# Performance work log

Hardware: AMD Instinct MI355X
Metric: run time of the kernel (lower is better)

Reference implementation:

```python
import jax, jax.numpy as jnp
import numpy as np

D_MODEL = 1024
N_HEADS = 16
HEAD_DIM = D_MODEL // N_HEADS
SEQ_LEN = 2048
BATCH = 4


def setup_inputs() -> dict:
    key = jax.random.key(0)
    k1, k2, k3 = jax.random.split(key, 3)
    x = jax.random.normal(k1, (BATCH, SEQ_LEN, D_MODEL), dtype=jnp.float32)
    # Linear weights stored as [in, out] so y = x @ W (equivalent to torch x @ W.T)
    w_qkv = jax.random.normal(k2, (D_MODEL, 3 * D_MODEL), dtype=jnp.float32) * (D_MODEL ** -0.5)
    w_proj = jax.random.normal(k3, (D_MODEL, D_MODEL), dtype=jnp.float32) * (D_MODEL ** -0.5)
    return {"x": x, "w_qkv": w_qkv, "w_proj": w_proj}


def reference(x, w_qkv, w_proj):
    B, T, C = x.shape
    qkv = x @ w_qkv  # [B, T, 3C]
    q, k, v = jnp.split(qkv, 3, axis=-1)
    # [B, H, T, hd]
    q = q.reshape(B, T, N_HEADS, HEAD_DIM).transpose(0, 2, 1, 3)
    k = k.reshape(B, T, N_HEADS, HEAD_DIM).transpose(0, 2, 1, 3)
    v = v.reshape(B, T, N_HEADS, HEAD_DIM).transpose(0, 2, 1, 3)
    scale = HEAD_DIM ** -0.5
    attn = jnp.einsum("bhqd,bhkd->bhqk", q, k) * scale  # [B, H, T, T]
    causal = jnp.tril(jnp.ones((T, T), dtype=bool))
    attn = jnp.where(causal, attn, -jnp.inf)
    attn = jax.nn.softmax(attn, axis=-1)
    out = jnp.einsum("bhqk,bhkd->bhqd", attn, v)  # [B, H, T, hd]
    out = out.transpose(0, 2, 1, 3).reshape(B, T, C)
    return out @ w_proj
```

## Files before the change

kernel.cpp:

```cpp
#include <hip/hip_runtime.h>
#include <stdint.h>


typedef __bf16 bf16x8 __attribute__((ext_vector_type(8)));
typedef float f32x4 __attribute__((ext_vector_type(4)));
typedef unsigned short u16x8 __attribute__((ext_vector_type(8)));

#define DEVINL static __device__ __forceinline__

DEVINL unsigned short f2b(float f) {
  __bf16 h = (__bf16)f;
  return __builtin_bit_cast(unsigned short, h);
}

DEVINL void gld16(const void* g, void* l) {
  __builtin_amdgcn_global_load_lds(
      (const __attribute__((address_space(1))) void*)g,
      (__attribute__((address_space(3))) void*)l, 16, 0, 0);
}

DEVINL f32x4 mfma16(bf16x8 a, bf16x8 b, f32x4 c) {
  return __builtin_amdgcn_mfma_f32_16x16x32_bf16(a, b, c, 0, 0, 0);
}

#define SCHED_FENCE() __builtin_amdgcn_sched_barrier(0)

__global__ __launch_bounds__(256) void k_cast_bf16(const float* __restrict__ in,
                                                   unsigned short* __restrict__ out,
                                                   int n8) {
  int i = blockIdx.x * 256 + threadIdx.x;
  if (i >= n8) return;
  const float4* p = (const float4*)in + (size_t)i * 2;
  float4 a = p[0], b = p[1];
  u16x8 o;
  o[0] = f2b(a.x); o[1] = f2b(a.y); o[2] = f2b(a.z); o[3] = f2b(a.w);
  o[4] = f2b(b.x); o[5] = f2b(b.y); o[6] = f2b(b.z); o[7] = f2b(b.w);
  *(u16x8*)(out + (size_t)i * 8) = o;
}

__global__ __launch_bounds__(256) void k_transpose_w(const float* __restrict__ in,
                                                     unsigned short* __restrict__ out,
                                                     int R, int C) {
  __shared__ float t[64][65];
  int ci = blockIdx.x * 64, ri = blockIdx.y * 64;
  int tid = threadIdx.x;
#pragma unroll
  for (int j = 0; j < 4; ++j) {
    int c = tid + j * 256;
    int row = c >> 4;
    int col = (c & 15) * 4;
    float4 v = *(const float4*)(in + (size_t)(ri + row) * C + ci + col);
    t[row][col] = v.x; t[row][col + 1] = v.y; t[row][col + 2] = v.z; t[row][col + 3] = v.w;
  }
  __syncthreads();
  int cc = tid >> 2;
  int seg = (tid & 3) * 16;
  u16x8 o0, o1;
#pragma unroll
  for (int j = 0; j < 8; ++j) o0[j] = f2b(t[seg + j][cc]);
#pragma unroll
  for (int j = 0; j < 8; ++j) o1[j] = f2b(t[seg + 8 + j][cc]);
  unsigned short* dst = out + (size_t)(ci + cc) * R + ri + seg;
  *(u16x8*)dst = o0;
  *(u16x8*)(dst + 8) = o1;
}

__global__ __launch_bounds__(512, 4)
void k_gemmQKV(const unsigned short* __restrict__ A,
               const unsigned short* __restrict__ Bt,
               unsigned short* __restrict__ qo,
               unsigned short* __restrict__ ko,
               unsigned short* __restrict__ vo,
               float qscale) {
  const int K = 1024, N = 3072;
  __shared__ unsigned short As[3][256 * 32];
  __shared__ unsigned short Bs[3][128 * 32];
  int tid = threadIdx.x;
  int w = tid >> 6, lane = tid & 63, l15 = lane & 15, l4 = lane >> 4;
  int nwg = gridDim.x;
  int gx = N >> 7;
  int lin = blockIdx.x;
  int nx = nwg >> 3, rr = nwg & 7;
  int xcd = lin & 7, idx = lin >> 3;
  int wgid = (xcd < rr ? xcd * (nx + 1) : rr * (nx + 1) + (xcd - rr) * nx) + idx;
  int bn = wgid % gx, bm = wgid / gx;
  int wr = (w >> 1) * 64, wc = (w & 1) * 64;
  f32x4 acc[4][4];
#pragma unroll
  for (int i = 0; i < 4; ++i)
#pragma unroll
    for (int j = 0; j < 4; ++j) acc[i][j] = (f32x4){0.f, 0.f, 0.f, 0.f};
  const char* Ab = (const char*)(A + (size_t)bm * 256 * K);
  const char* Bb = (const char*)(Bt + (size_t)bn * 128 * K);
  const size_t Kb2 = (size_t)K * 2;
  int LbA0 = tid * 16, LbA1 = (tid + 512) * 16, LbB = tid * 16;
  int NA0 = LbA0 ^ (((LbA0 >> 7) & 3) << 4);
  int NA1 = LbA1 ^ (((LbA1 >> 7) & 3) << 4);
  int NB  = LbB  ^ (((LbB  >> 7) & 3) << 4);
  int rA0 = NA0 >> 6, oA0 = NA0 & 63;
  int rA1 = NA1 >> 6, oA1 = NA1 & 63;
  int rB  = NB  >> 6, oB  = NB  & 63;

  auto stage = [&](int kt, int buf) {
    gld16(Ab + (size_t)rA0 * Kb2 + kt * 2 + oA0, (char*)As[buf] + LbA0);
    gld16(Ab + (size_t)rA1 * Kb2 + kt * 2 + oA1, (char*)As[buf] + LbA1);
    gld16(Bb + (size_t)rB  * Kb2 + kt * 2 + oB,  (char*)Bs[buf] + LbB);
  };

  const int nkt = K >> 5;
  stage(0, 0);
  stage(32, 1);
  SCHED_FENCE();
  for (int t = 0; t < nkt; ++t) {
    int cur = t - (t / 3) * 3;
    if (t) {
      SCHED_FENCE();
      __builtin_amdgcn_s_barrier();
      SCHED_FENCE();
    }
    if (t + 2 < nkt) {
      int nb = (t + 2) - ((t + 2) / 3) * 3;
      stage((t + 2) * 32, nb);
      SCHED_FENCE();
      asm volatile("s_waitcnt vmcnt(6)" ::: "memory");
    } else if (t + 1 < nkt) {
      SCHED_FENCE();
      asm volatile("s_waitcnt vmcnt(3)" ::: "memory");
    } else {
      SCHED_FENCE();
      asm volatile("s_waitcnt vmcnt(0)" ::: "memory");
    }
    SCHED_FENCE();
    __builtin_amdgcn_s_barrier();
    SCHED_FENCE();
    const char* Ac = (const char*)As[cur];
    const char* Bc = (const char*)Bs[cur];
    bf16x8 af[4], bfr[4];
#pragma unroll
    for (int m = 0; m < 4; ++m) {
      int nat = (wr + m * 16 + l15) * 64 + l4 * 16;
      af[m] = *(const bf16x8*)(Ac + (nat ^ (((nat >> 7) & 3) << 4)));
    }
#pragma unroll
    for (int n = 0; n < 4; ++n) {
      int nat = (wc + n * 16 + l15) * 64 + l4 * 16;
      bfr[n] = *(const bf16x8*)(Bc + (nat ^ (((nat >> 7) & 3) << 4)));
    }
    __builtin_amdgcn_s_setprio(1);
#pragma unroll
    for (int m = 0; m < 4; ++m)
#pragma unroll
      for (int n = 0; n < 4; ++n)
        acc[m][n] = mfma16(af[m], bfr[n], acc[m][n]);
    __builtin_amdgcn_s_setprio(0);
  }
#pragma unroll
  for (int m = 0; m < 4; ++m) {
    int grow0 = bm * 256 + wr + m * 16 + l4 * 4;
#pragma unroll
    for (int n = 0; n < 4; ++n) {
      int gcol = bn * 128 + wc + n * 16 + l15;
      int which = gcol >> 10, rem = gcol & 1023;
      int h = rem >> 6, d = rem & 63;
      int b = grow0 >> 11, t0 = grow0 & 2047;
      if (which == 2) {
        uint32_t lo = (uint32_t)f2b(acc[m][n][0]) | ((uint32_t)f2b(acc[m][n][1]) << 16);
        uint32_t hi = (uint32_t)f2b(acc[m][n][2]) | ((uint32_t)f2b(acc[m][n][3]) << 16);
        size_t off = (((size_t)(b * 16 + h)) * 64 + d) * 2048 + t0;
        *(uint2*)(vo + off) = make_uint2(lo, hi);
      } else {
        size_t off = (((size_t)(b * 16 + h)) * 2048 + t0) * 64 + d;
#pragma unroll
        for (int r = 0; r < 4; ++r) {
          float val = acc[m][n][r];
          if (which == 0) qo[off + (size_t)r * 64] = f2b(val * qscale);
          else            ko[off + (size_t)r * 64] = f2b(val);
        }
      }
    }
  }
}

__global__ __launch_bounds__(256) void k_gemm_out(const unsigned short* __restrict__ A,
                                                  const unsigned short* __restrict__ Bt,
                                                  int M, int N, int K,
                                                  float* __restrict__ Cf) {
  __shared__ unsigned short As[3][128 * 32];
  __shared__ unsigned short Bs[3][128 * 32];
  int tid = threadIdx.x;
  int w = tid >> 6, lane = tid & 63, l15 = lane & 15, l4 = lane >> 4;
  int nwg = gridDim.x;
  int gx = N >> 7;
  int lin = blockIdx.x;
  int nx = nwg >> 3, rr = nwg & 7;
  int xcd = lin & 7, idx = lin >> 3;
  int wgid = (xcd < rr ? xcd * (nx + 1) : rr * (nx + 1) + (xcd - rr) * nx) + idx;
  int bn = wgid % gx, bm = wgid / gx;
  int wr = (w >> 1) * 64, wc = (w & 1) * 64;
  f32x4 acc[4][4];
#pragma unroll
  for (int i = 0; i < 4; ++i)
#pragma unroll
    for (int j = 0; j < 4; ++j) acc[i][j] = (f32x4){0.f, 0.f, 0.f, 0.f};
  const char* Ab = (const char*)(A + (size_t)bm * 128 * K);
  const char* Bb = (const char*)(Bt + (size_t)bn * 128 * K);
  int Lb0 = tid * 16, Lb1 = (tid + 256) * 16;
  int Nb0 = Lb0 ^ (((Lb0 >> 7) & 3) << 4);
  int Nb1 = Lb1 ^ (((Lb1 >> 7) & 3) << 4);
  int rA0 = Nb0 >> 6, o0 = Nb0 & 63;
  int rA1 = Nb1 >> 6, o1 = Nb1 & 63;

  auto stage = [&](int kt, int buf) {
    gld16(Ab + ((size_t)rA0 * K + kt) * 2 + o0, (char*)As[buf] + Lb0);
    gld16(Bb + ((size_t)rA0 * K + kt) * 2 + o0, (char*)Bs[buf] + Lb0);
    gld16(Ab + ((size_t)rA1 * K + kt) * 2 + o1, (char*)As[buf] + Lb1);
    gld16(Bb + ((size_t)rA1 * K + kt) * 2 + o1, (char*)Bs[buf] + Lb1);
  };

  const int nkt = K >> 5;
  stage(0, 0);
  stage(32, 1);
  SCHED_FENCE();
  for (int t = 0; t < nkt; ++t) {
    int cur = t - (t / 3) * 3;
    if (t) {
      SCHED_FENCE();
      __builtin_amdgcn_s_barrier();
      SCHED_FENCE();
    }
    if (t + 2 < nkt) {
      int nb = (t + 2) - ((t + 2) / 3) * 3;
      stage((t + 2) * 32, nb);
      SCHED_FENCE();
      asm volatile("s_waitcnt vmcnt(8)" ::: "memory");
    } else if (t + 1 < nkt) {
      SCHED_FENCE();
      asm volatile("s_waitcnt vmcnt(4)" ::: "memory");
    } else {
      SCHED_FENCE();
      asm volatile("s_waitcnt vmcnt(0)" ::: "memory");
    }
    SCHED_FENCE();
    __builtin_amdgcn_s_barrier();
    SCHED_FENCE();
    const char* Ac = (const char*)As[cur];
    const char* Bc = (const char*)Bs[cur];
    bf16x8 af[4], bfr[4];
#pragma unroll
    for (int m = 0; m < 4; ++m) {
      int nat = (wr + m * 16 + l15) * 64 + l4 * 16;
      af[m] = *(const bf16x8*)(Ac + (nat ^ (((nat >> 7) & 3) << 4)));
    }
#pragma unroll
    for (int n = 0; n < 4; ++n) {
      int nat = (wc + n * 16 + l15) * 64 + l4 * 16;
      bfr[n] = *(const bf16x8*)(Bc + (nat ^ (((nat >> 7) & 3) << 4)));
    }
    __builtin_amdgcn_s_setprio(1);
#pragma unroll
    for (int m = 0; m < 4; ++m)
#pragma unroll
      for (int n = 0; n < 4; ++n)
        acc[m][n] = mfma16(af[m], bfr[n], acc[m][n]);
    __builtin_amdgcn_s_setprio(0);
  }
#pragma unroll
  for (int m = 0; m < 4; ++m) {
    int grow0 = bm * 128 + wr + m * 16 + l4 * 4;
#pragma unroll
    for (int n = 0; n < 4; ++n) {
      int gcol = bn * 128 + wc + n * 16 + l15;
#pragma unroll
      for (int r = 0; r < 4; ++r)
        Cf[(size_t)(grow0 + r) * N + gcol] = acc[m][n][r];
    }
  }
}

__global__ __launch_bounds__(512) void k_attn(const unsigned short* __restrict__ Q,
                                              const unsigned short* __restrict__ Kt,
                                              const unsigned short* __restrict__ Vt,
                                              unsigned short* __restrict__ AO) {
  __shared__ unsigned short Ks[2][4096];
  __shared__ unsigned short Vs[2][4096];
  __shared__ unsigned short Ps[8192];
  int tid = threadIdx.x;
  int w = tid >> 6, lane = tid & 63, l15 = lane & 15, l4 = lane >> 4;
  int lin = blockIdx.x;
  int xcd = lin & 7, jj = lin >> 3;
  int bh = xcd * 8 + (jj & 7);
  int p = jj >> 3;
  const char* Kb = (const char*)(Kt + (size_t)bh * 2048 * 64);
  const char* Vb = (const char*)(Vt + (size_t)bh * 64 * 2048);
  const int swp = (l15 & 7) << 4;
  char* Pw = (char*)Ps + w * 2048;
  int b = bh >> 4, h = bh & 15;

  int Lb0 = tid * 16;
  int Nb0 = Lb0 ^ (((Lb0 >> 7) & 7) << 4);
  int d0 = Nb0 >> 7, in0 = Nb0 & 127;

  auto stage = [&](int t, int buf) {
    size_t kv0 = (size_t)t * 64;
    gld16(Kb + kv0 * 128 + Nb0, (char*)Ks[buf] + Lb0);
    gld16(Vb + (size_t)d0 * 4096 + kv0 * 2 + in0, (char*)Vs[buf] + Lb0);
  };

  auto run = [&](int qi) {
    int q0 = qi * 128;
    const unsigned short* Qb = Q + ((size_t)bh * 2048 + q0 + w * 16) * 64;
    bf16x8 qf0 = *(const bf16x8*)((const char*)Qb + l15 * 128 + l4 * 16);
    bf16x8 qf1 = *(const bf16x8*)((const char*)Qb + l15 * 128 + 64 + l4 * 16);
    f32x4 o[4];
#pragma unroll
    for (int i = 0; i < 4; ++i) o[i] = (f32x4){0.f, 0.f, 0.f, 0.f};
    float mrow = -1e30f, lrow = 0.f;
    const int ntiles = 2 * qi + 2;
    const int qgmin = q0 + w * 16;
    const int qg = qgmin + l15;
    SCHED_FENCE();
    __builtin_amdgcn_s_barrier();
    SCHED_FENCE();
    stage(0, 0);
    SCHED_FENCE();
    for (int it = 0; it < ntiles; ++it) {
      int cur = it & 1;
      if (it) {
        SCHED_FENCE();
        __builtin_amdgcn_s_barrier();
        SCHED_FENCE();
      }
      if (it + 1 < ntiles) {
        stage(it + 1, cur ^ 1);
        SCHED_FENCE();
        asm volatile("s_waitcnt vmcnt(2)" ::: "memory");
      } else {
        SCHED_FENCE();
        asm volatile("s_waitcnt vmcnt(0)" ::: "memory");
      }
      SCHED_FENCE();
      __builtin_amdgcn_s_barrier();
      SCHED_FENCE();
      if (it * 64 <= qgmin + 15) {
        const char* Kc = (const char*)Ks[cur];
        const char* Vc = (const char*)Vs[cur];
        f32x4 s[4];
        __builtin_amdgcn_s_setprio(1);
#pragma unroll
        for (int c = 0; c < 4; ++c) {
          int row = c * 16 + l15;
          int base = row * 128 + l4 * 16;
          int sw = (row & 7) << 4;
          bf16x8 k0 = *(const bf16x8*)(Kc + (base ^ sw));
          bf16x8 k1 = *(const bf16x8*)(Kc + ((base + 64) ^ sw));
          f32x4 t = mfma16(k0, qf0, (f32x4){0.f, 0.f, 0.f, 0.f});
          s[c] = mfma16(k1, qf1, t);
        }
        __builtin_amdgcn_s_setprio(0);
        if (it * 64 + 63 > qgmin) {
#pragma unroll
          for (int c = 0; c < 4; ++c) {
            int kvb = it * 64 + c * 16 + l4 * 4;
#pragma unroll
            for (int r = 0; r < 4; ++r)
              if (kvb + r > qg) s[c][r] = -1e30f;
          }
        }
        float mx = fmaxf(fmaxf(fmaxf(s[0][0], s[0][1]), fmaxf(s[0][2], s[0][3])),
                         fmaxf(fmaxf(s[1][0], s[1][1]), fmaxf(s[1][2], s[1][3])));
        mx = fmaxf(mx, fmaxf(fmaxf(fmaxf(s[2][0], s[2][1]), fmaxf(s[2][2], s[2][3])),
                             fmaxf(fmaxf(s[3][0], s[3][1]), fmaxf(s[3][2], s[3][3]))));
        mx = fmaxf(mx, __shfl_xor(mx, 16));
        mx = fmaxf(mx, __shfl_xor(mx, 32));
        float mn = fmaxf(mrow, mx);
        float corr = __builtin_amdgcn_exp2f(mrow - mn);
        mrow = mn;
        float rs = 0.f;
#pragma unroll
        for (int c = 0; c < 4; ++c) {
          float p0 = __builtin_amdgcn_exp2f(s[c][0] - mn);
          float p1 = __builtin_amdgcn_exp2f(s[c][1] - mn);
          float p2 = __builtin_amdgcn_exp2f(s[c][2] - mn);
          float p3 = __builtin_amdgcn_exp2f(s[c][3] - mn);
          rs += (p0 + p1) + (p2 + p3);
          uint32_t lo = (uint32_t)f2b(p0) | ((uint32_t)f2b(p1) << 16);
          uint32_t hi = (uint32_t)f2b(p2) | ((uint32_t)f2b(p3) << 16);
          *(uint2*)(Pw + ((l15 * 128 + c * 32 + l4 * 8) ^ swp)) = make_uint2(lo, hi);
        }
        rs += __shfl_xor(rs, 16);
        rs += __shfl_xor(rs, 32);
        lrow = lrow * corr + rs;
        float corr_r[4];
#pragma unroll
        for (int r = 0; r < 4; ++r) corr_r[r] = __shfl(corr, l4 * 4 + r);
#pragma unroll
        for (int dc = 0; dc < 4; ++dc)
#pragma unroll
          for (int r = 0; r < 4; ++r) o[dc][r] *= corr_r[r];
        bf16x8 pa[2];
#pragma unroll
        for (int kc = 0; kc < 2; ++kc)
          pa[kc] = *(const bf16x8*)(Pw + ((l15 * 128 + kc * 64 + l4 * 16) ^ swp));
        __builtin_amdgcn_s_setprio(1);
#pragma unroll
        for (int dc = 0; dc < 4; ++dc) {
#pragma unroll
          for (int kc = 0; kc < 2; ++kc) {
            int vrow = dc * 16 + l15;
            int vnat = vrow * 128 + kc * 64 + l4 * 16;
            bf16x8 vb = *(const bf16x8*)(Vc + (vnat ^ ((vrow & 7) << 4)));
            o[dc] = mfma16(pa[kc], vb, o[dc]);
          }
        }
        __builtin_amdgcn_s_setprio(0);
      }
    }
    float inv[4];
#pragma unroll
    for (int r = 0; r < 4; ++r) inv[r] = 1.f / __shfl(lrow, l4 * 4 + r);
#pragma unroll
    for (int dc = 0; dc < 4; ++dc) {
#pragma unroll
      for (int r = 0; r < 4; ++r) {
        int t = q0 + w * 16 + l4 * 4 + r;
        AO[((size_t)(b * 2048 + t)) * 1024 + h * 64 + dc * 16 + l15] =
            f2b(o[dc][r] * inv[r]);
      }
    }
  };

  run(15 - p);
  run(p);
}

extern "C" void kernel_launch(void* const* d_in, const int* in_sizes, int n_in,
                              void* d_out, int out_size, void* d_ws, size_t ws_size,
                              hipStream_t stream) {
  const float* x      = (const float*)d_in[0];
  const float* w_qkv  = (const float*)d_in[1];
  const float* w_proj = (const float*)d_in[2];
  float* out = (float*)d_out;
  char* ws = (char*)d_ws;
  const size_t MB = 1024 * 1024;
  unsigned short* xb     = (unsigned short*)(ws);
  unsigned short* ao     = (unsigned short*)(ws);
  unsigned short* wqkvT  = (unsigned short*)(ws + 16 * MB);
  unsigned short* wprojT = (unsigned short*)(ws + 22 * MB);
  unsigned short* q      = (unsigned short*)(ws + 24 * MB);
  unsigned short* k      = (unsigned short*)(ws + 40 * MB);
  unsigned short* vT     = (unsigned short*)(ws + 56 * MB);

  k_cast_bf16<<<4096, 256, 0, stream>>>(x, xb, 1048576);
  k_transpose_w<<<dim3(48, 16), 256, 0, stream>>>(w_qkv, wqkvT, 1024, 3072);
  k_transpose_w<<<dim3(16, 16), 256, 0, stream>>>(w_proj, wprojT, 1024, 1024);
  const float qscale = 0.125f * 1.44269504088896f;
  k_gemmQKV<<<768, 512, 0, stream>>>(xb, wqkvT, q, k, vT, qscale);
  k_attn<<<512, 512, 0, stream>>>(q, k, vT, ao);
  k_gemm_out<<<512, 256, 0, stream>>>(ao, wprojT, 8192, 1024, 1024, out);
}
```

Measured before the change: 178.4 us.

## Merge prep kernels into one launch and split attention into one q-block per workgroup

```diff
diff --git a/kernel.cpp b/kernel.cpp
--- a/kernel.cpp
+++ b/kernel.cpp
@@ -25,25 +25,37 @@
 
 #define SCHED_FENCE() __builtin_amdgcn_sched_barrier(0)
 
-__global__ __launch_bounds__(256) void k_cast_bf16(const float* __restrict__ in,
-                                                   unsigned short* __restrict__ out,
-                                                   int n8) {
-  int i = blockIdx.x * 256 + threadIdx.x;
-  if (i >= n8) return;
-  const float4* p = (const float4*)in + (size_t)i * 2;
-  float4 a = p[0], b = p[1];
-  u16x8 o;
-  o[0] = f2b(a.x); o[1] = f2b(a.y); o[2] = f2b(a.z); o[3] = f2b(a.w);
-  o[4] = f2b(b.x); o[5] = f2b(b.y); o[6] = f2b(b.z); o[7] = f2b(b.w);
-  *(u16x8*)(out + (size_t)i * 8) = o;
-}
-
-__global__ __launch_bounds__(256) void k_transpose_w(const float* __restrict__ in,
-                                                     unsigned short* __restrict__ out,
-                                                     int R, int C) {
+__global__ __launch_bounds__(256) void k_prep(const float* __restrict__ x,
+                                              unsigned short* __restrict__ xb,
+                                              const float* __restrict__ wqkv,
+                                              unsigned short* __restrict__ wqkvT,
+                                              const float* __restrict__ wproj,
+                                              unsigned short* __restrict__ wprojT) {
+  int blk = blockIdx.x;
+  int tid = threadIdx.x;
+  if (blk < 4096) {
+    int i = blk * 256 + tid;
+    const float4* p = (const float4*)x + (size_t)i * 2;
+    float4 a = p[0], b = p[1];
+    u16x8 o;
+    o[0] = f2b(a.x); o[1] = f2b(a.y); o[2] = f2b(a.z); o[3] = f2b(a.w);
+    o[4] = f2b(b.x); o[5] = f2b(b.y); o[6] = f2b(b.z); o[7] = f2b(b.w);
+    *(u16x8*)(xb + (size_t)i * 8) = o;
+    return;
+  }
   __shared__ float t[64][65];
-  int ci = blockIdx.x * 64, ri = blockIdx.y * 64;
-  int tid = threadIdx.x;
+  const float* in;
+  unsigned short* out;
+  int R, C, ci, ri;
+  if (blk < 4864) {
+    int bi = blk - 4096;
+    in = wqkv; out = wqkvT; R = 1024; C = 3072;
+    ci = (bi % 48) * 64; ri = (bi / 48) * 64;
+  } else {
+    int bi = blk - 4864;
+    in = wproj; out = wprojT; R = 1024; C = 1024;
+    ci = (bi % 16) * 64; ri = (bi / 16) * 64;
+  }
 #pragma unroll
   for (int j = 0; j < 4; ++j) {
     int c = tid + j * 256;
@@ -289,7 +301,7 @@
   int lin = blockIdx.x;
   int xcd = lin & 7, jj = lin >> 3;
   int bh = xcd * 8 + (jj & 7);
-  int p = jj >> 3;
+  int qi = 15 - (jj >> 3);
   const char* Kb = (const char*)(Kt + (size_t)bh * 2048 * 64);
   const char* Vb = (const char*)(Vt + (size_t)bh * 64 * 2048);
   const int swp = (l15 & 7) << 4;
@@ -306,131 +318,123 @@
     gld16(Vb + (size_t)d0 * 4096 + kv0 * 2 + in0, (char*)Vs[buf] + Lb0);
   };
 
-  auto run = [&](int qi) {
-    int q0 = qi * 128;
-    const unsigned short* Qb = Q + ((size_t)bh * 2048 + q0 + w * 16) * 64;
-    bf16x8 qf0 = *(const bf16x8*)((const char*)Qb + l15 * 128 + l4 * 16);
-    bf16x8 qf1 = *(const bf16x8*)((const char*)Qb + l15 * 128 + 64 + l4 * 16);
-    f32x4 o[4];
-#pragma unroll
-    for (int i = 0; i < 4; ++i) o[i] = (f32x4){0.f, 0.f, 0.f, 0.f};
-    float mrow = -1e30f, lrow = 0.f;
-    const int ntiles = 2 * qi + 2;
-    const int qgmin = q0 + w * 16;
-    const int qg = qgmin + l15;
+  int q0 = qi * 128;
+  const unsigned short* Qb = Q + ((size_t)bh * 2048 + q0 + w * 16) * 64;
+  bf16x8 qf0 = *(const bf16x8*)((const char*)Qb + l15 * 128 + l4 * 16);
+  bf16x8 qf1 = *(const bf16x8*)((const char*)Qb + l15 * 128 + 64 + l4 * 16);
+  f32x4 o[4];
+#pragma unroll
+  for (int i = 0; i < 4; ++i) o[i] = (f32x4){0.f, 0.f, 0.f, 0.f};
+  float mrow = -1e30f, lrow = 0.f;
+  const int ntiles = 2 * qi + 2;
+  const int qgmin = q0 + w * 16;
+  const int qg = qgmin + l15;
+  stage(0, 0);
+  SCHED_FENCE();
+  for (int it = 0; it < ntiles; ++it) {
+    int cur = it & 1;
+    if (it) {
+      SCHED_FENCE();
+      __builtin_amdgcn_s_barrier();
+      SCHED_FENCE();
+    }
+    if (it + 1 < ntiles) {
+      stage(it + 1, cur ^ 1);
+      SCHED_FENCE();
+      asm volatile("s_waitcnt vmcnt(2)" ::: "memory");
+    } else {
+      SCHED_FENCE();
+      asm volatile("s_waitcnt vmcnt(0)" ::: "memory");
+    }
     SCHED_FENCE();
     __builtin_amdgcn_s_barrier();
     SCHED_FENCE();
-    stage(0, 0);
-    SCHED_FENCE();
-    for (int it = 0; it < ntiles; ++it) {
-      int cur = it & 1;
-      if (it) {
-        SCHED_FENCE();
-        __builtin_amdgcn_s_barrier();
-        SCHED_FENCE();
+    if (it * 64 <= qgmin + 15) {
+      const char* Kc = (const char*)Ks[cur];
+      const char* Vc = (const char*)Vs[cur];
+      f32x4 s[4];
+      __builtin_amdgcn_s_setprio(1);
+#pragma unroll
+      for (int c = 0; c < 4; ++c) {
+        int row = c * 16 + l15;
+        int base = row * 128 + l4 * 16;
+        int sw = (row & 7) << 4;
+        bf16x8 k0 = *(const bf16x8*)(Kc + (base ^ sw));
+        bf16x8 k1 = *(const bf16x8*)(Kc + ((base + 64) ^ sw));
+        f32x4 t = mfma16(k0, qf0, (f32x4){0.f, 0.f, 0.f, 0.f});
+        s[c] = mfma16(k1, qf1, t);
       }
-      if (it + 1 < ntiles) {
-        stage(it + 1, cur ^ 1);
-        SCHED_FENCE();
-        asm volatile("s_waitcnt vmcnt(2)" ::: "memory");
-      } else {
-        SCHED_FENCE();
-        asm volatile("s_waitcnt vmcnt(0)" ::: "memory");
+      __builtin_amdgcn_s_setprio(0);
+      if (it * 64 + 63 > qgmin) {
+#pragma unroll
+        for (int c = 0; c < 4; ++c) {
+          int kvb = it * 64 + c * 16 + l4 * 4;
+#pragma unroll
+          for (int r = 0; r < 4; ++r)
+            if (kvb + r > qg) s[c][r] = -1e30f;
+        }
       }
-      SCHED_FENCE();
-      __builtin_amdgcn_s_barrier();
-      SCHED_FENCE();
-      if (it * 64 <= qgmin + 15) {
-        const char* Kc = (const char*)Ks[cur];
-        const char* Vc = (const char*)Vs[cur];
-        f32x4 s[4];
-        __builtin_amdgcn_s_setprio(1);
-#pragma unroll
-        for (int c = 0; c < 4; ++c) {
-          int row = c * 16 + l15;
-          int base = row * 128 + l4 * 16;
-          int sw = (row & 7) << 4;
-          bf16x8 k0 = *(const bf16x8*)(Kc + (base ^ sw));
-          bf16x8 k1 = *(const bf16x8*)(Kc + ((base + 64) ^ sw));
-          f32x4 t = mfma16(k0, qf0, (f32x4){0.f, 0.f, 0.f, 0.f});
-          s[c] = mfma16(k1, qf1, t);
+      float mx = fmaxf(fmaxf(fmaxf(s[0][0], s[0][1]), fmaxf(s[0][2], s[0][3])),
+                       fmaxf(fmaxf(s[1][0], s[1][1]), fmaxf(s[1][2], s[1][3])));
+      mx = fmaxf(mx, fmaxf(fmaxf(fmaxf(s[2][0], s[2][1]), fmaxf(s[2][2], s[2][3])),
+                           fmaxf(fmaxf(s[3][0], s[3][1]), fmaxf(s[3][2], s[3][3]))));
+      mx = fmaxf(mx, __shfl_xor(mx, 16));
+      mx = fmaxf(mx, __shfl_xor(mx, 32));
+      float mn = fmaxf(mrow, mx);
+      float corr = __builtin_amdgcn_exp2f(mrow - mn);
+      mrow = mn;
+      float rs = 0.f;
+#pragma unroll
+      for (int c = 0; c < 4; ++c) {
+        float p0 = __builtin_amdgcn_exp2f(s[c][0] - mn);
+        float p1 = __builtin_amdgcn_exp2f(s[c][1] - mn);
+        float p2 = __builtin_amdgcn_exp2f(s[c][2] - mn);
+        float p3 = __builtin_amdgcn_exp2f(s[c][3] - mn);
+        rs += (p0 + p1) + (p2 + p3);
+        uint32_t lo = (uint32_t)f2b(p0) | ((uint32_t)f2b(p1) << 16);
+        uint32_t hi = (uint32_t)f2b(p2) | ((uint32_t)f2b(p3) << 16);
+        *(uint2*)(Pw + ((l15 * 128 + c * 32 + l4 * 8) ^ swp)) = make_uint2(lo, hi);
+      }
+      rs += __shfl_xor(rs, 16);
+      rs += __shfl_xor(rs, 32);
+      lrow = lrow * corr + rs;
+      float corr_r[4];
+#pragma unroll
+      for (int r = 0; r < 4; ++r) corr_r[r] = __shfl(corr, l4 * 4 + r);
+#pragma unroll
+      for (int dc = 0; dc < 4; ++dc)
+#pragma unroll
+        for (int r = 0; r < 4; ++r) o[dc][r] *= corr_r[r];
+      bf16x8 pa[2];
+#pragma unroll
+      for (int kc = 0; kc < 2; ++kc)
+        pa[kc] = *(const bf16x8*)(Pw + ((l15 * 128 + kc * 64 + l4 * 16) ^ swp));
+      __builtin_amdgcn_s_setprio(1);
+#pragma unroll
+      for (int dc = 0; dc < 4; ++dc) {
+#pragma unroll
+        for (int kc = 0; kc < 2; ++kc) {
+          int vrow = dc * 16 + l15;
+          int vnat = vrow * 128 + kc * 64 + l4 * 16;
+          bf16x8 vb = *(const bf16x8*)(Vc + (vnat ^ ((vrow & 7) << 4)));
+          o[dc] = mfma16(pa[kc], vb, o[dc]);
         }
-        __builtin_amdgcn_s_setprio(0);
-        if (it * 64 + 63 > qgmin) {
-#pragma unroll
-          for (int c = 0; c < 4; ++c) {
-            int kvb = it * 64 + c * 16 + l4 * 4;
-#pragma unroll
-            for (int r = 0; r < 4; ++r)
-              if (kvb + r > qg) s[c][r] = -1e30f;
-          }
-        }
-        float mx = fmaxf(fmaxf(fmaxf(s[0][0], s[0][1]), fmaxf(s[0][2], s[0][3])),
-                         fmaxf(fmaxf(s[1][0], s[1][1]), fmaxf(s[1][2], s[1][3])));
-        mx = fmaxf(mx, fmaxf(fmaxf(fmaxf(s[2][0], s[2][1]), fmaxf(s[2][2], s[2][3])),
-                             fmaxf(fmaxf(s[3][0], s[3][1]), fmaxf(s[3][2], s[3][3]))));
-        mx = fmaxf(mx, __shfl_xor(mx, 16));
-        mx = fmaxf(mx, __shfl_xor(mx, 32));
-        float mn = fmaxf(mrow, mx);
-        float corr = __builtin_amdgcn_exp2f(mrow - mn);
-        mrow = mn;
-        float rs = 0.f;
-#pragma unroll
-        for (int c = 0; c < 4; ++c) {
-          float p0 = __builtin_amdgcn_exp2f(s[c][0] - mn);
-          float p1 = __builtin_amdgcn_exp2f(s[c][1] - mn);
-          float p2 = __builtin_amdgcn_exp2f(s[c][2] - mn);
-          float p3 = __builtin_amdgcn_exp2f(s[c][3] - mn);
-          rs += (p0 + p1) + (p2 + p3);
-          uint32_t lo = (uint32_t)f2b(p0) | ((uint32_t)f2b(p1) << 16);
-          uint32_t hi = (uint32_t)f2b(p2) | ((uint32_t)f2b(p3) << 16);
-          *(uint2*)(Pw + ((l15 * 128 + c * 32 + l4 * 8) ^ swp)) = make_uint2(lo, hi);
-        }
-        rs += __shfl_xor(rs, 16);
-        rs += __shfl_xor(rs, 32);
-        lrow = lrow * corr + rs;
-        float corr_r[4];
-#pragma unroll
-        for (int r = 0; r < 4; ++r) corr_r[r] = __shfl(corr, l4 * 4 + r);
-#pragma unroll
-        for (int dc = 0; dc < 4; ++dc)
-#pragma unroll
-          for (int r = 0; r < 4; ++r) o[dc][r] *= corr_r[r];
-        bf16x8 pa[2];
-#pragma unroll
-        for (int kc = 0; kc < 2; ++kc)
-          pa[kc] = *(const bf16x8*)(Pw + ((l15 * 128 + kc * 64 + l4 * 16) ^ swp));
-        __builtin_amdgcn_s_setprio(1);
-#pragma unroll
-        for (int dc = 0; dc < 4; ++dc) {
-#pragma unroll
-          for (int kc = 0; kc < 2; ++kc) {
-            int vrow = dc * 16 + l15;
-            int vnat = vrow * 128 + kc * 64 + l4 * 16;
-            bf16x8 vb = *(const bf16x8*)(Vc + (vnat ^ ((vrow & 7) << 4)));
-            o[dc] = mfma16(pa[kc], vb, o[dc]);
-          }
-        }
-        __builtin_amdgcn_s_setprio(0);
       }
-    }
-    float inv[4];
-#pragma unroll
-    for (int r = 0; r < 4; ++r) inv[r] = 1.f / __shfl(lrow, l4 * 4 + r);
-#pragma unroll
-    for (int dc = 0; dc < 4; ++dc) {
-#pragma unroll
-      for (int r = 0; r < 4; ++r) {
-        int t = q0 + w * 16 + l4 * 4 + r;
-        AO[((size_t)(b * 2048 + t)) * 1024 + h * 64 + dc * 16 + l15] =
-            f2b(o[dc][r] * inv[r]);
-      }
-    }
-  };
-
-  run(15 - p);
-  run(p);
+      __builtin_amdgcn_s_setprio(0);
+    }
+  }
+  float inv[4];
+#pragma unroll
+  for (int r = 0; r < 4; ++r) inv[r] = 1.f / __shfl(lrow, l4 * 4 + r);
+#pragma unroll
+  for (int dc = 0; dc < 4; ++dc) {
+#pragma unroll
+    for (int r = 0; r < 4; ++r) {
+      int t = q0 + w * 16 + l4 * 4 + r;
+      AO[((size_t)(b * 2048 + t)) * 1024 + h * 64 + dc * 16 + l15] =
+          f2b(o[dc][r] * inv[r]);
+    }
+  }
 }
 
 extern "C" void kernel_launch(void* const* d_in, const int* in_sizes, int n_in,
@@ -450,11 +454,9 @@
   unsigned short* k      = (unsigned short*)(ws + 40 * MB);
   unsigned short* vT     = (unsigned short*)(ws + 56 * MB);
 
-  k_cast_bf16<<<4096, 256, 0, stream>>>(x, xb, 1048576);
-  k_transpose_w<<<dim3(48, 16), 256, 0, stream>>>(w_qkv, wqkvT, 1024, 3072);
-  k_transpose_w<<<dim3(16, 16), 256, 0, stream>>>(w_proj, wprojT, 1024, 1024);
   const float qscale = 0.125f * 1.44269504088896f;
+  k_prep<<<5120, 256, 0, stream>>>(x, xb, w_qkv, wqkvT, w_proj, wprojT);
   k_gemmQKV<<<768, 512, 0, stream>>>(xb, wqkvT, q, k, vT, qscale);
-  k_attn<<<512, 512, 0, stream>>>(q, k, vT, ao);
+  k_attn<<<1024, 512, 0, stream>>>(q, k, vT, ao);
   k_gemm_out<<<512, 256, 0, stream>>>(ao, wprojT, 8192, 1024, 1024, out);
 }
```

Result: faster. 174.1 us (median of 3 runs) (-2.4%).
